# Performance work log

Hardware: AMD Instinct MI355X
Metric: run time of the kernel (lower is better)

The kernel has to match this reference:

```python
import jax, jax.numpy as jnp
import numpy as np

L1 = 1536
L2 = 15
L3 = 64
COUNT = 8
B = 16384


def setup_inputs() -> dict:
    key = jax.random.key(0)
    ks = jax.random.split(key, 10)
    d_in = 2 * L1 // 2  # 1536
    s1 = 1.0 / np.sqrt(d_in)
    s2 = 1.0 / np.sqrt(2 * L2)
    s3 = 1.0 / np.sqrt(L3)
    return {
        "x": jax.random.normal(ks[0], (B, d_in), dtype=jnp.float32),
        "ls_indices": jax.random.randint(ks[1], (B,), 0, COUNT, dtype=jnp.int32),
        "W1": jax.random.uniform(ks[2], (COUNT * (L2 + 1), d_in), jnp.float32, -s1, s1),
        "b1": jax.random.uniform(ks[3], (COUNT * (L2 + 1),), jnp.float32, -s1, s1),
        "Wf": jax.random.uniform(ks[4], (L2 + 1, d_in), jnp.float32, -s1, s1),
        "bf": jax.random.uniform(ks[5], (L2 + 1,), jnp.float32, -s1, s1),
        "W2": jax.random.uniform(ks[6], (COUNT * L3, 2 * L2), jnp.float32, -s2, s2),
        "b2": jax.random.uniform(ks[7], (COUNT * L3,), jnp.float32, -s2, s2),
        "Wo": jax.random.uniform(ks[8], (COUNT, L3), jnp.float32, -s3, s3),
        "bo": jax.random.uniform(ks[9], (COUNT,), jnp.float32, -s3, s3),
    }


def reference(x, ls_indices, W1, b1, Wf, bf, W2, b2, Wo, bo):
    count = Wo.shape[0]
    n = x.shape[0]
    idx = ls_indices[:, None, None]  # [B,1,1] selects the per-sample stack

    # l1: all stacks, then gather selected stack row per sample
    l1s = (x @ W1.T + b1).reshape(n, count, L2 + 1)          # [B, count, 16]
    l1f = x @ Wf.T + bf                                       # [B, 16]
    l1c = jnp.take_along_axis(l1s, idx, axis=1)[:, 0]         # [B, 16]

    l1c_, l1c_out = l1c[:, :L2], l1c[:, L2:]                  # [B,15], [B,1]
    l1f_, l1f_out = l1f[:, :L2], l1f[:, L2:]
    l1x = l1c_ + l1f_
    # squared-clipped-ReLU concat: [pow(x,2)*127/128, x] clamped to [0,1]
    l1x = jnp.clip(jnp.concatenate([l1x * l1x * (127.0 / 128.0), l1x], axis=1), 0.0, 1.0)  # [B,30]

    l2s = (l1x @ W2.T + b2).reshape(n, count, L3)             # [B, count, 64]
    l2c = jnp.take_along_axis(l2s, idx, axis=1)[:, 0]         # [B, 64]
    l2x = jnp.clip(l2c, 0.0, 1.0)

    l3s = (l2x @ Wo.T + bo).reshape(n, count, 1)              # [B, count, 1]
    l3c = jnp.take_along_axis(l3s, idx, axis=1)[:, 0]         # [B, 1]
    return l3c + l1f_out + l1c_out
```

## Files before the change

kernel.cpp:

```cpp
#include <hip/hip_runtime.h>
#include <hip/hip_bf16.h>
#include <stdint.h>

#define L1DIM 1536
#define NOUT  144
#define MTILE 16
#define BK    128
#define NITER (L1DIM / BK)

typedef __bf16 bf16;
typedef __bf16 bf16x8 __attribute__((ext_vector_type(8)));
typedef float  floatx4 __attribute__((ext_vector_type(4)));

__global__ void pack_weights(const float* __restrict__ W1,
                             const float* __restrict__ Wf,
                             bf16* __restrict__ pw) {
    int t = blockIdx.x * blockDim.x + threadIdx.x;
    if (t >= NOUT * 192) return;
    int n = t / 192;
    int o = t % 192;
    const float* src = (n < 128) ? (W1 + (size_t)n * L1DIM + o * 8)
                                 : (Wf + (size_t)(n - 128) * L1DIM + o * 8);
    float4 s0 = ((const float4*)src)[0];
    float4 s1 = ((const float4*)src)[1];
    bf16x8 v;
    v[0] = (bf16)s0.x; v[1] = (bf16)s0.y; v[2] = (bf16)s0.z; v[3] = (bf16)s0.w;
    v[4] = (bf16)s1.x; v[5] = (bf16)s1.y; v[6] = (bf16)s1.z; v[7] = (bf16)s1.w;
    *(bf16x8*)(pw + ((size_t)o * NOUT + n) * 8) = v;
}

__device__ __forceinline__ void gload_lds16(const void* g, void* l) {
    __builtin_amdgcn_global_load_lds(
        (const __attribute__((address_space(1))) void*)g,
        (__attribute__((address_space(3))) void*)l, 16, 0, 0);
}

__device__ __forceinline__ bf16x8 cvt8(float4 a, float4 b) {
    bf16x8 r;
    r[0] = (bf16)a.x; r[1] = (bf16)a.y; r[2] = (bf16)a.z; r[3] = (bf16)a.w;
    r[4] = (bf16)b.x; r[5] = (bf16)b.y; r[6] = (bf16)b.z; r[7] = (bf16)b.w;
    return r;
}

__global__ __launch_bounds__(256, 4) void layerstacks_main(
    const float* __restrict__ x, const int* __restrict__ lsidx,
    const bf16* __restrict__ pw,
    const float* __restrict__ b1, const float* __restrict__ bf_,
    const float* __restrict__ W2, const float* __restrict__ b2,
    const float* __restrict__ Wo, const float* __restrict__ bo,
    float* __restrict__ out)
{
    __shared__ float la[2][MTILE * BK];
    __shared__ float ep4[4][MTILE][33];

    const int tid  = threadIdx.x;
    const int wv   = tid >> 6;
    const int ln   = tid & 63;
    const int quad = ln >> 4;
    const int lm   = ln & 15;
    const int ks   = wv;

    const int R0 = blockIdx.x * MTILE;

    const int sro = ln >> 5;
    const int sch = ln & 31;

    floatx4 acc[9];
#pragma unroll
    for (int i = 0; i < 9; i++) acc[i] = (floatx4){0.f, 0.f, 0.f, 0.f};

#define STAGE(buf, ki_)                                                        \
    {                                                                          \
        const int k0_ = (ki_) * BK;                                            \
        _Pragma("unroll")                                                      \
        for (int jj = 0; jj < 2; jj++) {                                       \
            const int j   = 2 * wv + jj;                                       \
            const int row = 2 * j + sro;                                       \
            const int cg  = sch ^ (row & 7);                                   \
            gload_lds16(x + (size_t)(R0 + row) * L1DIM + k0_ + cg * 4,         \
                        &la[buf][j * 2 * BK + sro * BK + sch * 4]);            \
        }                                                                      \
    }

    STAGE(0, 0)
    __syncthreads();

    const int c0 = ks * 8 + quad * 2;

    for (int ki = 0; ki < NITER; ki++) {
        const int cur = ki & 1;
        if (ki < NITER - 1) STAGE(cur ^ 1, ki + 1)

        const int row = lm;
        float4 a0 = *(const float4*)&la[cur][row * BK + ((c0)     ^ (row & 7)) * 4];
        float4 a1 = *(const float4*)&la[cur][row * BK + ((c0 + 1) ^ (row & 7)) * 4];
        bf16x8 af = cvt8(a0, a1);

        const bf16* bsl = pw + ((size_t)(ki * 16 + ks * 4 + quad) * NOUT) * 8;
#pragma unroll
        for (int t = 0; t < 9; t++) {
            bf16x8 bfrag = *(const bf16x8*)(bsl + ((size_t)(t * 16 + lm)) * 8);
            acc[t] = __builtin_amdgcn_mfma_f32_16x16x32_bf16(af, bfrag, acc[t], 0, 0, 0);
        }
        __syncthreads();
    }

    {
#pragma unroll
        for (int r = 0; r < 4; r++) {
            const int row = quad * 4 + r;
            const int bkt = lsidx[R0 + row];
            float c = acc[0][r];
#pragma unroll
            for (int t = 1; t < 8; t++) c = (bkt == t) ? acc[t][r] : c;
            ep4[ks][row][lm]      = c;
            ep4[ks][row][16 + lm] = acc[8][r];
        }
    }
    __syncthreads();

    {
        const int col = tid & 31;
        const int rr  = tid >> 5;
#pragma unroll
        for (int p = 0; p < 2; p++) {
            const int row = rr + p * 8;
            ep4[0][row][col] = ep4[0][row][col] + ep4[1][row][col]
                             + ep4[2][row][col] + ep4[3][row][col];
        }
    }
    __syncthreads();

    if (tid < 128) {
        const int er   = tid >> 3;
        const int sub  = tid & 7;
        const int grow = R0 + er;
        const int bkt  = lsidx[grow];

        const float l1c15 = ep4[0][er][15] + b1[bkt * 16 + 15];
        const float l1f15 = ep4[0][er][31] + bf_[15];

        float l1x[30];
#pragma unroll
        for (int j = 0; j < 15; j++) {
            float tj = (ep4[0][er][j] + b1[bkt * 16 + j]) + (ep4[0][er][16 + j] + bf_[j]);
            float sq = tj * tj * (127.0f / 128.0f);
            l1x[j]      = fminf(fmaxf(sq, 0.f), 1.f);
            l1x[15 + j] = fminf(fmaxf(tj, 0.f), 1.f);
        }

        float part = 0.f;
#pragma unroll
        for (int o = 0; o < 8; o++) {
            const int oi = bkt * 64 + sub * 8 + o;
            const float2* wrow = (const float2*)(W2 + oi * 30);
            float a = b2[oi];
#pragma unroll
            for (int j2 = 0; j2 < 15; j2++) {
                float2 w = wrow[j2];
                a += l1x[2 * j2] * w.x + l1x[2 * j2 + 1] * w.y;
            }
            a = fminf(fmaxf(a, 0.f), 1.f);
            part += a * Wo[oi];
        }
        part += __shfl_xor(part, 1);
        part += __shfl_xor(part, 2);
        part += __shfl_xor(part, 4);
        if (sub == 0) out[grow] = part + bo[bkt] + l1c15 + l1f15;
    }
}

extern "C" void kernel_launch(void* const* d_in, const int* in_sizes, int n_in,
                              void* d_out, int out_size, void* d_ws, size_t ws_size,
                              hipStream_t stream) {
    const float* x   = (const float*)d_in[0];
    const int*   idx = (const int*)  d_in[1];
    const float* W1  = (const float*)d_in[2];
    const float* b1  = (const float*)d_in[3];
    const float* Wf  = (const float*)d_in[4];
    const float* bf  = (const float*)d_in[5];
    const float* W2  = (const float*)d_in[6];
    const float* b2  = (const float*)d_in[7];
    const float* Wo  = (const float*)d_in[8];
    const float* bo  = (const float*)d_in[9];
    float* out = (float*)d_out;
    bf16*  pw  = (bf16*)d_ws;

    pack_weights<<<dim3((NOUT * 192 + 255) / 256), dim3(256), 0, stream>>>(W1, Wf, pw);
    layerstacks_main<<<dim3(16384 / MTILE), dim3(256), 0, stream>>>(
        x, idx, pw, b1, bf, W2, b2, Wo, bo, out);
}
```

Before: 182.0 us.

## Sort rows by layer-stack bucket so each tile computes only its stack

```diff
diff --git a/kernel.cpp b/kernel.cpp
--- a/kernel.cpp
+++ b/kernel.cpp
@@ -7,26 +7,78 @@
 #define MTILE 16
 #define BK    128
 #define NITER (L1DIM / BK)
+#define NBUF  4
+#define PERMN 16512
+#define GMAIN 1032
 
 typedef __bf16 bf16;
 typedef __bf16 bf16x8 __attribute__((ext_vector_type(8)));
 typedef float  floatx4 __attribute__((ext_vector_type(4)));
 
-__global__ void pack_weights(const float* __restrict__ W1,
-                             const float* __restrict__ Wf,
-                             bf16* __restrict__ pw) {
-    int t = blockIdx.x * blockDim.x + threadIdx.x;
-    if (t >= NOUT * 192) return;
-    int n = t / 192;
-    int o = t % 192;
-    const float* src = (n < 128) ? (W1 + (size_t)n * L1DIM + o * 8)
-                                 : (Wf + (size_t)(n - 128) * L1DIM + o * 8);
-    float4 s0 = ((const float4*)src)[0];
-    float4 s1 = ((const float4*)src)[1];
-    bf16x8 v;
-    v[0] = (bf16)s0.x; v[1] = (bf16)s0.y; v[2] = (bf16)s0.z; v[3] = (bf16)s0.w;
-    v[4] = (bf16)s1.x; v[5] = (bf16)s1.y; v[6] = (bf16)s1.z; v[7] = (bf16)s1.w;
-    *(bf16x8*)(pw + ((size_t)o * NOUT + n) * 8) = v;
+__global__ void k_pack_hist(const float* __restrict__ W1,
+                            const float* __restrict__ Wf,
+                            bf16* __restrict__ pw,
+                            const int* __restrict__ lsidx,
+                            int* __restrict__ perm,
+                            int* __restrict__ meta) {
+    const int gb = blockIdx.x;
+    if (gb < 108) {
+        int t = gb * 256 + threadIdx.x;
+        int n = t / 192;
+        int o = t % 192;
+        const float* src = (n < 128) ? (W1 + (size_t)n * L1DIM + o * 8)
+                                     : (Wf + (size_t)(n - 128) * L1DIM + o * 8);
+        float4 s0 = ((const float4*)src)[0];
+        float4 s1 = ((const float4*)src)[1];
+        bf16x8 v;
+        v[0] = (bf16)s0.x; v[1] = (bf16)s0.y; v[2] = (bf16)s0.z; v[3] = (bf16)s0.w;
+        v[4] = (bf16)s1.x; v[5] = (bf16)s1.y; v[6] = (bf16)s1.z; v[7] = (bf16)s1.w;
+        *(bf16x8*)(pw + ((size_t)o * NOUT + n) * 8) = v;
+    } else {
+        const int i  = (gb - 108) * 256 + threadIdx.x;
+        perm[i] = -1;
+        if (i < PERMN - 16384) perm[16384 + i] = -1;
+        const int mb = lsidx[i];
+        const int ln = threadIdx.x & 63;
+#pragma unroll
+        for (int b = 0; b < 8; b++) {
+            unsigned long long m = __ballot(mb == b);
+            if (m && ln == (__ffsll(m) - 1))
+                atomicAdd(&meta[1 + b], (int)__popcll(m));
+        }
+    }
+}
+
+__global__ void k_offsets(int* __restrict__ meta) {
+    if (threadIdx.x == 0 && blockIdx.x == 0) {
+        int o = 0;
+#pragma unroll
+        for (int b = 0; b < 8; b++) {
+            meta[9 + b] = o;
+            o += (meta[1 + b] + 15) & ~15;
+        }
+        meta[0] = o;
+    }
+}
+
+__global__ void k_scatter(const int* __restrict__ lsidx,
+                          int* __restrict__ perm,
+                          int* __restrict__ meta) {
+    const int i  = blockIdx.x * 256 + threadIdx.x;
+    const int mb = lsidx[i];
+    const int ln = threadIdx.x & 63;
+#pragma unroll
+    for (int b = 0; b < 8; b++) {
+        unsigned long long m = __ballot(mb == b);
+        if (mb == b) {
+            int leader = __ffsll(m) - 1;
+            int base = 0;
+            if (ln == leader) base = atomicAdd(&meta[9 + b], (int)__popcll(m));
+            base = __shfl(base, leader);
+            int pos = base + (int)__popcll(m & ((1ull << ln) - 1));
+            perm[pos] = i;
+        }
+    }
 }
 
 __device__ __forceinline__ void gload_lds16(const void* g, void* l) {
@@ -44,77 +96,93 @@
 
 __global__ __launch_bounds__(256, 4) void layerstacks_main(
     const float* __restrict__ x, const int* __restrict__ lsidx,
-    const bf16* __restrict__ pw,
+    const bf16* __restrict__ pw, const int* __restrict__ perm,
+    const int* __restrict__ meta,
     const float* __restrict__ b1, const float* __restrict__ bf_,
     const float* __restrict__ W2, const float* __restrict__ b2,
     const float* __restrict__ Wo, const float* __restrict__ bo,
     float* __restrict__ out)
 {
-    __shared__ float la[2][MTILE * BK];
-    __shared__ float ep4[4][MTILE][33];
+    __shared__ float la[NBUF][MTILE * BK];
 
     const int tid  = threadIdx.x;
     const int wv   = tid >> 6;
     const int ln   = tid & 63;
     const int quad = ln >> 4;
     const int lm   = ln & 15;
-    const int ks   = wv;
 
     const int R0 = blockIdx.x * MTILE;
+    if (R0 >= meta[0]) return;
+
+    const int bkt = lsidx[perm[R0]];
 
     const int sro = ln >> 5;
     const int sch = ln & 31;
-
-    floatx4 acc[9];
-#pragma unroll
-    for (int i = 0; i < 9; i++) acc[i] = (floatx4){0.f, 0.f, 0.f, 0.f};
-
-#define STAGE(buf, ki_)                                                        \
-    {                                                                          \
-        const int k0_ = (ki_) * BK;                                            \
-        _Pragma("unroll")                                                      \
-        for (int jj = 0; jj < 2; jj++) {                                       \
-            const int j   = 2 * wv + jj;                                       \
-            const int row = 2 * j + sro;                                       \
-            const int cg  = sch ^ (row & 7);                                   \
-            gload_lds16(x + (size_t)(R0 + row) * L1DIM + k0_ + cg * 4,         \
-                        &la[buf][j * 2 * BK + sro * BK + sch * 4]);            \
-        }                                                                      \
-    }
-
-    STAGE(0, 0)
+    const int r0r = 4 * wv + sro;
+    const int r1r = 4 * wv + 2 + sro;
+    int pr0 = perm[R0 + r0r]; if (pr0 < 0) pr0 = 0;
+    int pr1 = perm[R0 + r1r]; if (pr1 < 0) pr1 = 0;
+    const float* g0 = x + (size_t)pr0 * L1DIM + ((sch ^ (r0r & 7)) << 2);
+    const float* g1 = x + (size_t)pr1 * L1DIM + ((sch ^ (r1r & 7)) << 2);
+
+#define STAGE(buf_, ki_)                                                \
+    {                                                                   \
+        gload_lds16(g0 + (size_t)(ki_) * BK, &la[buf_][r0r * BK + sch * 4]); \
+        gload_lds16(g1 + (size_t)(ki_) * BK, &la[buf_][r1r * BK + sch * 4]); \
+    }
+
+#define BLOAD(ki_, slot_)                                               \
+    {                                                                   \
+        const bf16* bb = pw + (size_t)((ki_) * 16 + wv * 4 + quad) * (NOUT * 8); \
+        bs[slot_][0] = *(const bf16x8*)(bb + (bkt * 16 + lm) * 8);      \
+        bs[slot_][1] = *(const bf16x8*)(bb + (128 + lm) * 8);           \
+    }
+
+    bf16x8  bs[3][2];
+    floatx4 acc0 = (floatx4){0.f, 0.f, 0.f, 0.f};
+    floatx4 acc1 = (floatx4){0.f, 0.f, 0.f, 0.f};
+
+    const int c0 = wv * 8 + quad * 2;
+
+    STAGE(0, 0) BLOAD(0, 0)
+    STAGE(1, 1) BLOAD(1, 1)
+
+#pragma unroll
+    for (int ki = 0; ki < NITER; ki++) {
+        if (ki == NITER - 1) asm volatile("s_waitcnt vmcnt(2)" ::: "memory");
+        else                 asm volatile("s_waitcnt vmcnt(6)" ::: "memory");
+        __builtin_amdgcn_s_barrier();
+        __builtin_amdgcn_sched_barrier(0);
+
+        const int row = lm;
+        float4 a0 = *(const float4*)&la[ki & 3][row * BK + ((c0)     ^ (row & 7)) * 4];
+        float4 a1 = *(const float4*)&la[ki & 3][row * BK + ((c0 + 1) ^ (row & 7)) * 4];
+
+        if (ki < NITER - 2) { STAGE((ki + 2) & 3, ki + 2) BLOAD(ki + 2, (ki + 2) % 3) }
+
+        bf16x8 af = cvt8(a0, a1);
+        acc0 = __builtin_amdgcn_mfma_f32_16x16x32_bf16(af, bs[ki % 3][0], acc0, 0, 0, 0);
+        acc1 = __builtin_amdgcn_mfma_f32_16x16x32_bf16(af, bs[ki % 3][1], acc1, 0, 0, 0);
+    }
+
+    float* sm = (float*)la;
+
     __syncthreads();
-
-    const int c0 = ks * 8 + quad * 2;
-
-    for (int ki = 0; ki < NITER; ki++) {
-        const int cur = ki & 1;
-        if (ki < NITER - 1) STAGE(cur ^ 1, ki + 1)
-
-        const int row = lm;
-        float4 a0 = *(const float4*)&la[cur][row * BK + ((c0)     ^ (row & 7)) * 4];
-        float4 a1 = *(const float4*)&la[cur][row * BK + ((c0 + 1) ^ (row & 7)) * 4];
-        bf16x8 af = cvt8(a0, a1);
-
-        const bf16* bsl = pw + ((size_t)(ki * 16 + ks * 4 + quad) * NOUT) * 8;
-#pragma unroll
-        for (int t = 0; t < 9; t++) {
-            bf16x8 bfrag = *(const bf16x8*)(bsl + ((size_t)(t * 16 + lm)) * 8);
-            acc[t] = __builtin_amdgcn_mfma_f32_16x16x32_bf16(af, bfrag, acc[t], 0, 0, 0);
-        }
-        __syncthreads();
-    }
 
     {
 #pragma unroll
         for (int r = 0; r < 4; r++) {
             const int row = quad * 4 + r;
-            const int bkt = lsidx[R0 + row];
-            float c = acc[0][r];
-#pragma unroll
-            for (int t = 1; t < 8; t++) c = (bkt == t) ? acc[t][r] : c;
-            ep4[ks][row][lm]      = c;
-            ep4[ks][row][16 + lm] = acc[8][r];
+            sm[(wv * 16 + row) * 33 + lm]      = acc0[r];
+            sm[(wv * 16 + row) * 33 + 16 + lm] = acc1[r];
+        }
+    }
+    {
+        const float* w2src = W2 + (size_t)bkt * 64 * 30;
+        for (int i = tid; i < 1920; i += 256) sm[2112 + i] = w2src[i];
+        if (tid < 64) {
+            sm[4032 + tid] = Wo[bkt * 64 + tid];
+            sm[4096 + tid] = b2[bkt * 64 + tid];
         }
     }
     __syncthreads();
@@ -125,49 +193,52 @@
 #pragma unroll
         for (int p = 0; p < 2; p++) {
             const int row = rr + p * 8;
-            ep4[0][row][col] = ep4[0][row][col] + ep4[1][row][col]
-                             + ep4[2][row][col] + ep4[3][row][col];
+            sm[row * 33 + col] = sm[row * 33 + col] + sm[528 + row * 33 + col]
+                               + sm[1056 + row * 33 + col] + sm[1584 + row * 33 + col];
         }
     }
     __syncthreads();
 
     if (tid < 128) {
-        const int er   = tid >> 3;
-        const int sub  = tid & 7;
-        const int grow = R0 + er;
-        const int bkt  = lsidx[grow];
-
-        const float l1c15 = ep4[0][er][15] + b1[bkt * 16 + 15];
-        const float l1f15 = ep4[0][er][31] + bf_[15];
-
-        float l1x[30];
-#pragma unroll
-        for (int j = 0; j < 15; j++) {
-            float tj = (ep4[0][er][j] + b1[bkt * 16 + j]) + (ep4[0][er][16 + j] + bf_[j]);
-            float sq = tj * tj * (127.0f / 128.0f);
-            l1x[j]      = fminf(fmaxf(sq, 0.f), 1.f);
-            l1x[15 + j] = fminf(fmaxf(tj, 0.f), 1.f);
-        }
-
-        float part = 0.f;
-#pragma unroll
-        for (int o = 0; o < 8; o++) {
-            const int oi = bkt * 64 + sub * 8 + o;
-            const float2* wrow = (const float2*)(W2 + oi * 30);
-            float a = b2[oi];
-#pragma unroll
-            for (int j2 = 0; j2 < 15; j2++) {
-                float2 w = wrow[j2];
-                a += l1x[2 * j2] * w.x + l1x[2 * j2 + 1] * w.y;
+        const int er  = tid >> 3;
+        const int sub = tid & 7;
+        const int pr  = perm[R0 + er];
+        if (pr >= 0) {
+            const float l1c15 = sm[er * 33 + 15] + b1[bkt * 16 + 15];
+            const float l1f15 = sm[er * 33 + 31] + bf_[15];
+
+            float l1x[30];
+#pragma unroll
+            for (int j = 0; j < 15; j++) {
+                float tj = (sm[er * 33 + j] + b1[bkt * 16 + j])
+                         + (sm[er * 33 + 16 + j] + bf_[j]);
+                float sq = tj * tj * (127.0f / 128.0f);
+                l1x[j]      = fminf(fmaxf(sq, 0.f), 1.f);
+                l1x[15 + j] = fminf(fmaxf(tj, 0.f), 1.f);
             }
-            a = fminf(fmaxf(a, 0.f), 1.f);
-            part += a * Wo[oi];
-        }
-        part += __shfl_xor(part, 1);
-        part += __shfl_xor(part, 2);
-        part += __shfl_xor(part, 4);
-        if (sub == 0) out[grow] = part + bo[bkt] + l1c15 + l1f15;
-    }
+
+            float part = 0.f;
+#pragma unroll
+            for (int o = 0; o < 8; o++) {
+                const int ol = sub * 8 + o;
+                const float* wrow = &sm[2112 + ol * 30];
+                float a = sm[4096 + ol];
+#pragma unroll
+                for (int j2 = 0; j2 < 15; j2++) {
+                    float2 w = *(const float2*)&wrow[2 * j2];
+                    a += l1x[2 * j2] * w.x + l1x[2 * j2 + 1] * w.y;
+                }
+                a = fminf(fmaxf(a, 0.f), 1.f);
+                part += a * sm[4032 + ol];
+            }
+            part += __shfl_xor(part, 1);
+            part += __shfl_xor(part, 2);
+            part += __shfl_xor(part, 4);
+            if (sub == 0) out[pr] = part + bo[bkt] + l1c15 + l1f15;
+        }
+    }
+#undef STAGE
+#undef BLOAD
 }
 
 extern "C" void kernel_launch(void* const* d_in, const int* in_sizes, int n_in,
@@ -184,9 +255,15 @@
     const float* Wo  = (const float*)d_in[8];
     const float* bo  = (const float*)d_in[9];
     float* out = (float*)d_out;
-    bf16*  pw  = (bf16*)d_ws;
-
-    pack_weights<<<dim3((NOUT * 192 + 255) / 256), dim3(256), 0, stream>>>(W1, Wf, pw);
-    layerstacks_main<<<dim3(16384 / MTILE), dim3(256), 0, stream>>>(
-        x, idx, pw, b1, bf, W2, b2, Wo, bo, out);
-}
+
+    bf16* pw   = (bf16*)d_ws;
+    int*  perm = (int*)((char*)d_ws + 442368);
+    int*  meta = perm + PERMN;
+
+    hipMemsetAsync(meta, 0, 17 * sizeof(int), stream);
+    k_pack_hist<<<dim3(172), dim3(256), 0, stream>>>(W1, Wf, pw, idx, perm, meta);
+    k_offsets <<<dim3(1),   dim3(64),  0, stream>>>(meta);
+    k_scatter <<<dim3(64),  dim3(256), 0, stream>>>(idx, perm, meta);
+    layerstacks_main<<<dim3(GMAIN), dim3(256), 0, stream>>>(
+        x, idx, pw, perm, meta, b1, bf, W2, b2, Wo, bo, out);
+}
```

After: 229.8 us. 1.26x slower.

## Load activations directly into registers and split K across waves without LDS

Applied to the files above, without the earlier changes.

```diff
diff --git a/kernel.cpp b/kernel.cpp
--- a/kernel.cpp
+++ b/kernel.cpp
@@ -5,18 +5,17 @@
 #define L1DIM 1536
 #define NOUT  144
 #define MTILE 16
-#define BK    128
-#define NITER (L1DIM / BK)
+#define NITER 12
 
 typedef __bf16 bf16;
 typedef __bf16 bf16x8 __attribute__((ext_vector_type(8)));
 typedef float  floatx4 __attribute__((ext_vector_type(4)));
 
-__global__ void pack_weights(const float* __restrict__ W1,
-                             const float* __restrict__ Wf,
-                             bf16* __restrict__ pw) {
-    int t = blockIdx.x * blockDim.x + threadIdx.x;
-    if (t >= NOUT * 192) return;
+__global__ __launch_bounds__(256) void pack_weights(
+    const float* __restrict__ W1, const float* __restrict__ Wf,
+    bf16* __restrict__ pw)
+{
+    int t = blockIdx.x * 256 + threadIdx.x;
     int n = t / 192;
     int o = t % 192;
     const float* src = (n < 128) ? (W1 + (size_t)n * L1DIM + o * 8)
@@ -27,12 +26,6 @@
     v[0] = (bf16)s0.x; v[1] = (bf16)s0.y; v[2] = (bf16)s0.z; v[3] = (bf16)s0.w;
     v[4] = (bf16)s1.x; v[5] = (bf16)s1.y; v[6] = (bf16)s1.z; v[7] = (bf16)s1.w;
     *(bf16x8*)(pw + ((size_t)o * NOUT + n) * 8) = v;
-}
-
-__device__ __forceinline__ void gload_lds16(const void* g, void* l) {
-    __builtin_amdgcn_global_load_lds(
-        (const __attribute__((address_space(1))) void*)g,
-        (__attribute__((address_space(3))) void*)l, 16, 0, 0);
 }
 
 __device__ __forceinline__ bf16x8 cvt8(float4 a, float4 b) {
@@ -50,7 +43,6 @@
     const float* __restrict__ Wo, const float* __restrict__ bo,
     float* __restrict__ out)
 {
-    __shared__ float la[2][MTILE * BK];
     __shared__ float ep4[4][MTILE][33];
 
     const int tid  = threadIdx.x;
@@ -58,64 +50,37 @@
     const int ln   = tid & 63;
     const int quad = ln >> 4;
     const int lm   = ln & 15;
-    const int ks   = wv;
 
     const int R0 = blockIdx.x * MTILE;
 
-    const int sro = ln >> 5;
-    const int sch = ln & 31;
+    const float* ax = x + (size_t)(R0 + lm) * L1DIM + wv * 384 + quad * 8;
 
     floatx4 acc[9];
 #pragma unroll
     for (int i = 0; i < 9; i++) acc[i] = (floatx4){0.f, 0.f, 0.f, 0.f};
 
-#define STAGE(buf, ki_)                                                        \
-    {                                                                          \
-        const int k0_ = (ki_) * BK;                                            \
-        _Pragma("unroll")                                                      \
-        for (int jj = 0; jj < 2; jj++) {                                       \
-            const int j   = 2 * wv + jj;                                       \
-            const int row = 2 * j + sro;                                       \
-            const int cg  = sch ^ (row & 7);                                   \
-            gload_lds16(x + (size_t)(R0 + row) * L1DIM + k0_ + cg * 4,         \
-                        &la[buf][j * 2 * BK + sro * BK + sch * 4]);            \
-        }                                                                      \
+#pragma unroll
+    for (int ki = 0; ki < NITER; ki++) {
+        float4 a0 = *(const float4*)(ax + ki * 32);
+        float4 a1 = *(const float4*)(ax + ki * 32 + 4);
+        const bf16* bsl = pw + (size_t)(wv * 48 + ki * 4 + quad) * (NOUT * 8);
+        bf16x8 af = cvt8(a0, a1);
+#pragma unroll
+        for (int t = 0; t < 9; t++) {
+            bf16x8 bfr = *(const bf16x8*)(bsl + (size_t)(t * 16 + lm) * 8);
+            acc[t] = __builtin_amdgcn_mfma_f32_16x16x32_bf16(af, bfr, acc[t], 0, 0, 0);
+        }
     }
 
-    STAGE(0, 0)
-    __syncthreads();
-
-    const int c0 = ks * 8 + quad * 2;
-
-    for (int ki = 0; ki < NITER; ki++) {
-        const int cur = ki & 1;
-        if (ki < NITER - 1) STAGE(cur ^ 1, ki + 1)
-
-        const int row = lm;
-        float4 a0 = *(const float4*)&la[cur][row * BK + ((c0)     ^ (row & 7)) * 4];
-        float4 a1 = *(const float4*)&la[cur][row * BK + ((c0 + 1) ^ (row & 7)) * 4];
-        bf16x8 af = cvt8(a0, a1);
-
-        const bf16* bsl = pw + ((size_t)(ki * 16 + ks * 4 + quad) * NOUT) * 8;
 #pragma unroll
-        for (int t = 0; t < 9; t++) {
-            bf16x8 bfrag = *(const bf16x8*)(bsl + ((size_t)(t * 16 + lm)) * 8);
-            acc[t] = __builtin_amdgcn_mfma_f32_16x16x32_bf16(af, bfrag, acc[t], 0, 0, 0);
-        }
-        __syncthreads();
-    }
-
-    {
+    for (int r = 0; r < 4; r++) {
+        const int row = quad * 4 + r;
+        const int bkt = lsidx[R0 + row];
+        float c = acc[0][r];
 #pragma unroll
-        for (int r = 0; r < 4; r++) {
-            const int row = quad * 4 + r;
-            const int bkt = lsidx[R0 + row];
-            float c = acc[0][r];
-#pragma unroll
-            for (int t = 1; t < 8; t++) c = (bkt == t) ? acc[t][r] : c;
-            ep4[ks][row][lm]      = c;
-            ep4[ks][row][16 + lm] = acc[8][r];
-        }
+        for (int t = 1; t < 8; t++) c = (bkt == t) ? acc[t][r] : c;
+        ep4[wv][row][lm]      = c;
+        ep4[wv][row][16 + lm] = acc[8][r];
     }
     __syncthreads();
 
@@ -143,7 +108,8 @@
         float l1x[30];
 #pragma unroll
         for (int j = 0; j < 15; j++) {
-            float tj = (ep4[0][er][j] + b1[bkt * 16 + j]) + (ep4[0][er][16 + j] + bf_[j]);
+            float tj = (ep4[0][er][j] + b1[bkt * 16 + j])
+                     + (ep4[0][er][16 + j] + bf_[j]);
             float sq = tj * tj * (127.0f / 128.0f);
             l1x[j]      = fminf(fmaxf(sq, 0.f), 1.f);
             l1x[15 + j] = fminf(fmaxf(tj, 0.f), 1.f);
@@ -186,7 +152,7 @@
     float* out = (float*)d_out;
     bf16*  pw  = (bf16*)d_ws;
 
-    pack_weights<<<dim3((NOUT * 192 + 255) / 256), dim3(256), 0, stream>>>(W1, Wf, pw);
+    pack_weights<<<dim3(108), dim3(256), 0, stream>>>(W1, Wf, pw);
     layerstacks_main<<<dim3(16384 / MTILE), dim3(256), 0, stream>>>(
         x, idx, pw, b1, bf, W2, b2, Wo, bo, out);
 }
```

After: 188.0 us. +3.3%, slower.
